# Kernel optimization log

Hardware: AMD Instinct MI355X
Metric: run time of the kernel (lower is better)

The kernel has to match this reference:

```python
import jax, jax.numpy as jnp
import numpy as np

B, N, D, H = 4, 2048, 1024, 16
DH = D // H


def setup_inputs() -> dict:
    key = jax.random.key(0)
    ks = jax.random.split(key, 9)
    s = 1.0 / np.sqrt(D)
    return {
        "x": jax.random.normal(ks[0], (B, N, D), dtype=jnp.float32),
        "Wq": jax.random.normal(ks[1], (D, D), dtype=jnp.float32) * s,
        "bq": jax.random.normal(ks[2], (D,), dtype=jnp.float32) * 0.01,
        "Wk": jax.random.normal(ks[3], (D, D), dtype=jnp.float32) * s,
        "bk": jax.random.normal(ks[4], (D,), dtype=jnp.float32) * 0.01,
        "Wv": jax.random.normal(ks[5], (D, D), dtype=jnp.float32) * s,
        "bv": jax.random.normal(ks[6], (D,), dtype=jnp.float32) * 0.01,
        "Wp": jax.random.normal(ks[7], (D, D), dtype=jnp.float32) * s,
        "bp": jax.random.normal(ks[8], (D,), dtype=jnp.float32) * 0.01,
    }


def reference(x, Wq, bq, Wk, bk, Wv, bv, Wp, bp):
    b, n, d = x.shape
    # torch Linear: x @ W.T + b; reshape to (b, h, n, dh)
    def heads(W, bias):
        y = jnp.einsum('bnd,ed->bne', x, W) + bias
        return y.reshape(b, n, H, DH).transpose(0, 2, 1, 3)
    q, k, v = heads(Wq, bq), heads(Wk, bk), heads(Wv, bv)
    # NOTE: source multiplies by sqrt(d_head) (bug in original), kept faithfully
    scale = jnp.sqrt(jnp.float32(DH))
    att = jnp.einsum('bhqd,bhkd->bhqk', q, k) * scale
    causal = jnp.triu(jnp.ones((n, n), dtype=bool), k=1)  # True above diagonal
    att = jnp.where(causal, -jnp.inf, att)
    att = jax.nn.softmax(att, axis=-1)
    # dropout is eval-mode identity
    out = jnp.einsum('bhqk,bhkd->bhqd', att, v)
    out = out.transpose(0, 2, 1, 3).reshape(b, n, d)
    return jnp.einsum('bnd,ed->bne', out, Wp) + bp
```

## Files before the change

### kernel.cpp

```cpp
#include <hip/hip_runtime.h>
#include <hip/hip_fp16.h>


typedef _Float16 half8 __attribute__((ext_vector_type(8)));
typedef _Float16 half4 __attribute__((ext_vector_type(4)));
typedef float f32x4 __attribute__((ext_vector_type(4)));
typedef unsigned int u32x4 __attribute__((ext_vector_type(4)));

#define DEV __device__ __forceinline__
#define MFMA16(a, b, c) __builtin_amdgcn_mfma_f32_16x16x32_f16(a, b, c, 0, 0, 0)

DEV void gload_lds16(const void* g, void* l) {
  __builtin_amdgcn_global_load_lds(
      (const __attribute__((address_space(1))) void*)g,
      (__attribute__((address_space(3))) void*)l, 16, 0, 0);
}

__global__ __launch_bounds__(256) void cast_all(
    const float* __restrict__ x, const float* __restrict__ Wq,
    const float* __restrict__ Wk, const float* __restrict__ Wv,
    const float* __restrict__ Wp, __half* __restrict__ xb,
    __half* __restrict__ wqkv, __half* __restrict__ wpb) {
  int i = blockIdx.x * 256 + threadIdx.x;
  const float* s;
  __half* d;
  int j;
  if (i < 1048576) {
    s = x; d = xb; j = i;
  } else {
    int k = i - 1048576;
    int sel = k >> 17;
    j = k & 131071;
    s = (sel == 0) ? Wq : (sel == 1) ? Wk : (sel == 2) ? Wv : Wp;
    d = (sel == 3) ? wpb : (wqkv + sel * 1048576);
  }
  const float4* sp = (const float4*)s + (size_t)j * 2;
  float4 a = sp[0], b = sp[1];
  half8 h;
  h[0] = (_Float16)a.x; h[1] = (_Float16)a.y; h[2] = (_Float16)a.z; h[3] = (_Float16)a.w;
  h[4] = (_Float16)b.x; h[5] = (_Float16)b.y; h[6] = (_Float16)b.z; h[7] = (_Float16)b.w;
  *((half8*)d + j) = h;
}

template <int MODE>
__global__ __launch_bounds__(256) void gemm128(
    const __half* __restrict__ A, const __half* __restrict__ Bm,
    const float* __restrict__ b0, const float* __restrict__ b1,
    const float* __restrict__ b2, __half* __restrict__ oh,
    __half* __restrict__ vtp, float* __restrict__ of) {
  const int m0 = blockIdx.y * 128;
  const int n0 = blockIdx.x * 128;
  const int tid = threadIdx.x;
  const int w = tid >> 6, lane = tid & 63;
  const int lr = lane & 15, lq = lane >> 4;
  const int wr = w >> 1, wc = w & 1;

  __shared__ alignas(16) __half As[128 * 64];
  __shared__ alignas(16) __half Bs[128 * 64];

  f32x4 acc[4][4] = {};

  const int arow = lane >> 3;
  const int acol = (lane & 7) * 8;
  const __half* Agp = A + ((size_t)m0 + w * 32 + arow) * 1024 + acol;
  const __half* Bgp = Bm + ((size_t)n0 + w * 32 + arow) * 1024 + acol;

  for (int kt = 0; kt < 16; ++kt) {
#pragma unroll
    for (int j = 0; j < 4; ++j) {
      gload_lds16(Agp + j * 8192 + kt * 64, As + (w * 4 + j) * 512);
      gload_lds16(Bgp + j * 8192 + kt * 64, Bs + (w * 4 + j) * 512);
    }
    __syncthreads();
#pragma unroll
    for (int s = 0; s < 2; ++s) {
      half8 af[4], bf[4];
#pragma unroll
      for (int i = 0; i < 4; ++i) {
        af[i] = *(const half8*)(As + (wr * 64 + i * 16 + lr) * 64 + s * 32 + lq * 8);
        bf[i] = *(const half8*)(Bs + (wc * 64 + i * 16 + lr) * 64 + s * 32 + lq * 8);
      }
#pragma unroll
      for (int mi = 0; mi < 4; ++mi)
#pragma unroll
        for (int ni = 0; ni < 4; ++ni)
          acc[mi][ni] = MFMA16(af[mi], bf[ni], acc[mi][ni]);
    }
    __syncthreads();
  }

  if (MODE == 0) {
#pragma unroll
    for (int ni = 0; ni < 4; ++ni) {
      int col = n0 + wc * 64 + ni * 16 + lr;
      int t = col >> 10, e = col & 1023;
      const float* bb = (t == 0) ? b0 : ((t == 1) ? b1 : b2);
      float bias = bb[e];
      int hh = e >> 6, dh = e & 63;
      if (t == 2) {
#pragma unroll
        for (int mi = 0; mi < 4; ++mi) {
          int row = m0 + wr * 64 + mi * 16 + lq * 4;
          int b_ = row >> 11, n = row & 2047;
          half4 h;
#pragma unroll
          for (int r = 0; r < 4; ++r) h[r] = (_Float16)(acc[mi][ni][r] + bias);
          *(half4*)(vtp + (size_t)(b_ * 16 + hh) * 131072 + (size_t)dh * 2048 + n) = h;
        }
      } else {
        float scale = (t == 0) ? 11.541560327111707f : 1.0f;
        __half* base = oh + (size_t)t * 8388608 + dh;
#pragma unroll
        for (int mi = 0; mi < 4; ++mi)
#pragma unroll
          for (int r = 0; r < 4; ++r) {
            int row = m0 + wr * 64 + mi * 16 + lq * 4 + r;
            int b_ = row >> 11, n = row & 2047;
            float v = (acc[mi][ni][r] + bias) * scale;
            base[(((size_t)(b_ * 16 + hh) * 2048 + n) * 64)] = __float2half(v);
          }
      }
    }
  } else {
#pragma unroll
    for (int ni = 0; ni < 4; ++ni) {
      int col = n0 + wc * 64 + ni * 16 + lr;
      float bias = b0[col];
#pragma unroll
      for (int mi = 0; mi < 4; ++mi)
#pragma unroll
        for (int r = 0; r < 4; ++r) {
          int row = m0 + wr * 64 + mi * 16 + lq * 4 + r;
          of[(size_t)row * 1024 + col] = acc[mi][ni][r] + bias;
        }
    }
  }
}

__global__ __launch_bounds__(256, 4) void attn128(const __half* __restrict__ Q,
                                                  const __half* __restrict__ K,
                                                  const __half* __restrict__ Vt,
                                                  __half* __restrict__ O) {
  const int wg = blockIdx.x;
  const int bh = wg & 63;
  const int a2 = wg >> 6, g4 = a2 >> 2, pos = a2 & 3;
  const int qt = (g4 == 0) ? 15 - pos
               : (g4 == 1) ? 8 + pos
               : (g4 == 2) ? 7 - pos
                           : pos;
  const int b = bh >> 4, h = bh & 15;
  const int tid = threadIdx.x;
  const int w = tid >> 6, lane = tid & 63;
  const int lr = lane & 15, lq = lane >> 4;
  const int hi = lane >> 5;
  const int sAl = (lane & 15) | ((lane & 16) << 1);
  const int sBl = sAl + 16;

  __shared__ alignas(16) __half Ks[2][4096];
  __shared__ alignas(16) __half Vs[2][4096];

  const __half* Kb = K + (size_t)bh * 131072;
  const __half* Vb = Vt + (size_t)bh * 131072;

  const int srow0 = tid >> 3;
  const int srow1 = srow0 + 32;
  const int scol = ((tid & 7) ^ (srow0 & 7)) * 8;

#define STAGE(t, buf)                                                          \
  do {                                                                         \
    gload_lds16(Kb + (size_t)((t)*64 + srow0) * 64 + scol, Ks[buf] + tid * 8); \
    gload_lds16(Kb + (size_t)((t)*64 + srow1) * 64 + scol,                     \
                Ks[buf] + 2048 + tid * 8);                                     \
    gload_lds16(Vb + (size_t)srow0 * 2048 + (t)*64 + scol, Vs[buf] + tid * 8); \
    gload_lds16(Vb + (size_t)srow1 * 2048 + (t)*64 + scol,                     \
                Vs[buf] + 2048 + tid * 8);                                     \
  } while (0)

  const int q0 = qt * 128;
  const int ktend = 2 * qt + 2;
  const int rmin = q0 + w * 32;
  const int myqa = rmin + lr;
  const int myqb = rmin + 16 + lr;

  const __half* Qpa = Q + ((size_t)bh * 2048 + rmin) * 64;
  half8 qf0a = *(const half8*)(Qpa + lr * 64 + lq * 8);
  half8 qf1a = *(const half8*)(Qpa + lr * 64 + 32 + lq * 8);
  half8 qf0b = *(const half8*)(Qpa + (16 + lr) * 64 + lq * 8);
  half8 qf1b = *(const half8*)(Qpa + (16 + lr) * 64 + 32 + lq * 8);

  f32x4 oacca[4] = {}, oaccb[4] = {};
  float ma = -INFINITY, la = 0.f, mb = -INFINITY, lb = 0.f;

  STAGE(0, 0);
  asm volatile("" ::: "memory");

  auto smgrp = [&](f32x4* sacc, float& m, float& l, int myq, int k0,
                   bool needmask, f32x4* oacc, half8& pa0, half8& pa1) {
    if (needmask) {
#pragma unroll
      for (int nt = 0; nt < 4; ++nt)
#pragma unroll
        for (int r = 0; r < 4; ++r) {
          int key = k0 + nt * 16 + lq * 4 + r;
          if (key > myq) sacc[nt][r] = -INFINITY;
        }
    }
    float rm = fmaxf(fmaxf(fmaxf(sacc[0][0], sacc[0][1]),
                           fmaxf(sacc[0][2], sacc[0][3])),
                     fmaxf(fmaxf(sacc[1][0], sacc[1][1]),
                           fmaxf(sacc[1][2], sacc[1][3])));
    rm = fmaxf(rm, fmaxf(fmaxf(fmaxf(sacc[2][0], sacc[2][1]),
                               fmaxf(sacc[2][2], sacc[2][3])),
                         fmaxf(fmaxf(sacc[3][0], sacc[3][1]),
                               fmaxf(sacc[3][2], sacc[3][3]))));
    rm = fmaxf(rm, __shfl_xor(rm, 16));
    rm = fmaxf(rm, __shfl_xor(rm, 32));
    if (__any(rm > m + 8.f)) {
      float mn = fmaxf(m, rm);
      float al = __builtin_amdgcn_exp2f(m - mn);
      m = mn;
      l *= al;
      float al4[4];
#pragma unroll
      for (int r = 0; r < 4; ++r) al4[r] = __shfl(al, lq * 4 + r);
#pragma unroll
      for (int dt = 0; dt < 4; ++dt)
#pragma unroll
        for (int r = 0; r < 4; ++r) oacc[dt][r] *= al4[r];
    }
    float ps = 0.f;
#pragma unroll
    for (int nt = 0; nt < 4; ++nt) {
      float p0 = __builtin_amdgcn_exp2f(sacc[nt][0] - m);
      float p1 = __builtin_amdgcn_exp2f(sacc[nt][1] - m);
      float p2 = __builtin_amdgcn_exp2f(sacc[nt][2] - m);
      float p3 = __builtin_amdgcn_exp2f(sacc[nt][3] - m);
      sacc[nt][0] = p0; sacc[nt][1] = p1;
      sacc[nt][2] = p2; sacc[nt][3] = p3;
      ps += (p0 + p1) + (p2 + p3);
    }
    ps += __shfl_xor(ps, 16);
    ps += __shfl_xor(ps, 32);
    l += ps;
    unsigned ph[8];
#pragma unroll
    for (int nt = 0; nt < 4; ++nt) {
      __half2 pha = __floats2half2_rn(sacc[nt][0], sacc[nt][1]);
      __half2 phb = __floats2half2_rn(sacc[nt][2], sacc[nt][3]);
      ph[2 * nt] = *(unsigned*)&pha;
      ph[2 * nt + 1] = *(unsigned*)&phb;
    }
    u32x4 fa, fb;
    {
      unsigned t0, t1;
      t0 = __shfl((int)ph[0], sAl); t1 = __shfl((int)ph[2], sAl);
      fa[0] = hi ? t1 : t0;
      t0 = __shfl((int)ph[1], sAl); t1 = __shfl((int)ph[3], sAl);
      fa[1] = hi ? t1 : t0;
      t0 = __shfl((int)ph[0], sBl); t1 = __shfl((int)ph[2], sBl);
      fa[2] = hi ? t1 : t0;
      t0 = __shfl((int)ph[1], sBl); t1 = __shfl((int)ph[3], sBl);
      fa[3] = hi ? t1 : t0;
      t0 = __shfl((int)ph[4], sAl); t1 = __shfl((int)ph[6], sAl);
      fb[0] = hi ? t1 : t0;
      t0 = __shfl((int)ph[5], sAl); t1 = __shfl((int)ph[7], sAl);
      fb[1] = hi ? t1 : t0;
      t0 = __shfl((int)ph[4], sBl); t1 = __shfl((int)ph[6], sBl);
      fb[2] = hi ? t1 : t0;
      t0 = __shfl((int)ph[5], sBl); t1 = __shfl((int)ph[7], sBl);
      fb[3] = hi ? t1 : t0;
    }
    pa0 = *(half8*)&fa;
    pa1 = *(half8*)&fb;
  };

  for (int kt = 0; kt < ktend; ++kt) {
    const int cur = kt & 1;
    const int k0 = kt * 64;
    if (kt + 1 < ktend) {
      STAGE(kt + 1, cur ^ 1);
      asm volatile("s_waitcnt vmcnt(4)" ::: "memory");
    } else {
      asm volatile("s_waitcnt vmcnt(0)" ::: "memory");
    }
    __builtin_amdgcn_s_barrier();
    asm volatile("" ::: "memory");

    const char* Kc = (const char*)Ks[cur];
    const char* Vc = (const char*)Vs[cur];
    if (k0 <= rmin + 31) {
      f32x4 sa[4] = {}, sb[4] = {};
      __builtin_amdgcn_s_setprio(1);
#pragma unroll
      for (int nt = 0; nt < 4; ++nt) {
        int row = nt * 16 + lr;
        half8 kb0 = *(const half8*)(Kc + ((row * 128 + lq * 16) ^ ((row & 7) << 4)));
        half8 kb1 = *(const half8*)(Kc + ((row * 128 + 64 + lq * 16) ^ ((row & 7) << 4)));
        sa[nt] = MFMA16(kb0, qf0a, sa[nt]);
        sa[nt] = MFMA16(kb1, qf1a, sa[nt]);
        sb[nt] = MFMA16(kb0, qf0b, sb[nt]);
        sb[nt] = MFMA16(kb1, qf1b, sb[nt]);
      }
      __builtin_amdgcn_s_setprio(0);

      half8 paa0, paa1, pab0, pab1;
      smgrp(sa, ma, la, myqa, k0, k0 + 63 > rmin, oacca, paa0, paa1);
      smgrp(sb, mb, lb, myqb, k0, k0 + 63 > rmin + 16, oaccb, pab0, pab1);

      __builtin_amdgcn_s_setprio(1);
#pragma unroll
      for (int dt = 0; dt < 4; ++dt) {
        int row = dt * 16 + lr;
        half8 vb0 = *(const half8*)(Vc + ((row * 128 + lq * 16) ^ ((row & 7) << 4)));
        half8 vb1 = *(const half8*)(Vc + ((row * 128 + 64 + lq * 16) ^ ((row & 7) << 4)));
        oacca[dt] = MFMA16(paa0, vb0, oacca[dt]);
        oacca[dt] = MFMA16(paa1, vb1, oacca[dt]);
        oaccb[dt] = MFMA16(pab0, vb0, oaccb[dt]);
        oaccb[dt] = MFMA16(pab1, vb1, oaccb[dt]);
      }
      __builtin_amdgcn_s_setprio(0);
    }
    asm volatile("s_waitcnt lgkmcnt(0)" ::: "memory");
    __builtin_amdgcn_s_barrier();
    asm volatile("" ::: "memory");
  }

  float linva = 1.0f / la, linvb = 1.0f / lb;
  float inva[4], invb[4];
#pragma unroll
  for (int r = 0; r < 4; ++r) {
    inva[r] = __shfl(linva, lq * 4 + r);
    invb[r] = __shfl(linvb, lq * 4 + r);
  }
  __half* Opa = O + ((size_t)b * 2048 + rmin) * 1024 + h * 64;
#pragma unroll
  for (int dt = 0; dt < 4; ++dt)
#pragma unroll
    for (int r = 0; r < 4; ++r) {
      Opa[(size_t)(lq * 4 + r) * 1024 + dt * 16 + lr] =
          __float2half(oacca[dt][r] * inva[r]);
      Opa[(size_t)(16 + lq * 4 + r) * 1024 + dt * 16 + lr] =
          __float2half(oaccb[dt][r] * invb[r]);
    }
#undef STAGE
}

extern "C" void kernel_launch(void* const* d_in, const int* in_sizes, int n_in,
                              void* d_out, int out_size, void* d_ws,
                              size_t ws_size, hipStream_t stream) {
  const float* x = (const float*)d_in[0];
  const float* Wq = (const float*)d_in[1];
  const float* bq = (const float*)d_in[2];
  const float* Wk = (const float*)d_in[3];
  const float* bk = (const float*)d_in[4];
  const float* Wv = (const float*)d_in[5];
  const float* bv = (const float*)d_in[6];
  const float* Wp = (const float*)d_in[7];
  const float* bp = (const float*)d_in[8];

  char* ws = (char*)d_ws;
  const size_t XB = 0;
  const size_t WQKV = XB + 16777216;
  const size_t WPB = WQKV + 6291456;
  const size_t QKV = WPB + 2097152;
  const size_t VT = QKV + 50331648;
  const size_t OB = VT + 16777216;

  __half* xb = (__half*)(ws + XB);
  __half* wqkv = (__half*)(ws + WQKV);
  __half* wpb = (__half*)(ws + WPB);
  __half* qkv = (__half*)(ws + QKV);
  __half* vt = (__half*)(ws + VT);
  __half* ob = (__half*)(ws + OB);

  cast_all<<<6144, 256, 0, stream>>>(x, Wq, Wk, Wv, Wp, xb, wqkv, wpb);

  gemm128<0><<<dim3(24, 64), 256, 0, stream>>>(xb, wqkv, bq, bk, bv, qkv, vt,
                                               nullptr);
  attn128<<<dim3(1024), 256, 0, stream>>>(qkv, qkv + 8388608, vt, ob);
  gemm128<1><<<dim3(8, 64), 256, 0, stream>>>(ob, wpb, bp, nullptr, nullptr,
                                              nullptr, nullptr, (float*)d_out);
}
```

Before: 190.8 us.

## Widen attention waves to 64 query rows with 128-thread blocks

The attention kernel now uses 2-wave, 128-thread blocks, and each wave processes 64 query rows as four 16-row groups instead of 32 rows. This doubles the reuse of each K/V fragment read from LDS, and each thread stages twice as many K/V chunks. Groups lying entirely above the causal diagonal skip their MFMAs and softmax. The row-sum cross-lane reduction moves from every tile to the epilogue. The interleaved query-tile schedule is replaced by a plain heavy-first order, and the larger per-wave accumulator state raises register pressure and may lower occupancy.

```diff
diff --git a/kernel.cpp b/kernel.cpp
--- a/kernel.cpp
+++ b/kernel.cpp
@@ -137,17 +137,12 @@
   }
 }
 
-__global__ __launch_bounds__(256, 4) void attn128(const __half* __restrict__ Q,
-                                                  const __half* __restrict__ K,
-                                                  const __half* __restrict__ Vt,
-                                                  __half* __restrict__ O) {
+__global__ __launch_bounds__(128, 2) void attn_quad(
+    const __half* __restrict__ Q, const __half* __restrict__ K,
+    const __half* __restrict__ Vt, __half* __restrict__ O) {
   const int wg = blockIdx.x;
   const int bh = wg & 63;
-  const int a2 = wg >> 6, g4 = a2 >> 2, pos = a2 & 3;
-  const int qt = (g4 == 0) ? 15 - pos
-               : (g4 == 1) ? 8 + pos
-               : (g4 == 2) ? 7 - pos
-                           : pos;
+  const int qt = 15 - (wg >> 6);
   const int b = bh >> 4, h = bh & 15;
   const int tid = threadIdx.x;
   const int w = tid >> 6, lane = tid & 63;
@@ -162,34 +157,40 @@
   const __half* Kb = K + (size_t)bh * 131072;
   const __half* Vb = Vt + (size_t)bh * 131072;
 
-  const int srow0 = tid >> 3;
-  const int srow1 = srow0 + 32;
-  const int scol = ((tid & 7) ^ (srow0 & 7)) * 8;
+  const int srow = tid >> 3;
+  const int scol = ((tid & 7) ^ (srow & 7)) * 8;
 
 #define STAGE(t, buf)                                                          \
   do {                                                                         \
-    gload_lds16(Kb + (size_t)((t)*64 + srow0) * 64 + scol, Ks[buf] + tid * 8); \
-    gload_lds16(Kb + (size_t)((t)*64 + srow1) * 64 + scol,                     \
-                Ks[buf] + 2048 + tid * 8);                                     \
-    gload_lds16(Vb + (size_t)srow0 * 2048 + (t)*64 + scol, Vs[buf] + tid * 8); \
-    gload_lds16(Vb + (size_t)srow1 * 2048 + (t)*64 + scol,                     \
-                Vs[buf] + 2048 + tid * 8);                                     \
+    const __half* kg = Kb + (size_t)((t)*64 + srow) * 64 + scol;               \
+    const __half* vg = Vb + (size_t)srow * 2048 + (t)*64 + scol;               \
+    gload_lds16(kg, Ks[buf] + tid * 8);                                        \
+    gload_lds16(kg + 16 * 64, Ks[buf] + 1024 + tid * 8);                       \
+    gload_lds16(kg + 32 * 64, Ks[buf] + 2048 + tid * 8);                       \
+    gload_lds16(kg + 48 * 64, Ks[buf] + 3072 + tid * 8);                       \
+    gload_lds16(vg, Vs[buf] + tid * 8);                                        \
+    gload_lds16(vg + 16 * 2048, Vs[buf] + 1024 + tid * 8);                     \
+    gload_lds16(vg + 32 * 2048, Vs[buf] + 2048 + tid * 8);                     \
+    gload_lds16(vg + 48 * 2048, Vs[buf] + 3072 + tid * 8);                     \
   } while (0)
 
   const int q0 = qt * 128;
   const int ktend = 2 * qt + 2;
-  const int rmin = q0 + w * 32;
-  const int myqa = rmin + lr;
-  const int myqb = rmin + 16 + lr;
+  const int rmin = q0 + w * 64;
 
   const __half* Qpa = Q + ((size_t)bh * 2048 + rmin) * 64;
   half8 qf0a = *(const half8*)(Qpa + lr * 64 + lq * 8);
   half8 qf1a = *(const half8*)(Qpa + lr * 64 + 32 + lq * 8);
   half8 qf0b = *(const half8*)(Qpa + (16 + lr) * 64 + lq * 8);
   half8 qf1b = *(const half8*)(Qpa + (16 + lr) * 64 + 32 + lq * 8);
-
-  f32x4 oacca[4] = {}, oaccb[4] = {};
+  half8 qf0c = *(const half8*)(Qpa + (32 + lr) * 64 + lq * 8);
+  half8 qf1c = *(const half8*)(Qpa + (32 + lr) * 64 + 32 + lq * 8);
+  half8 qf0d = *(const half8*)(Qpa + (48 + lr) * 64 + lq * 8);
+  half8 qf1d = *(const half8*)(Qpa + (48 + lr) * 64 + 32 + lq * 8);
+
+  f32x4 oacca[4] = {}, oaccb[4] = {}, oaccc[4] = {}, oaccd[4] = {};
   float ma = -INFINITY, la = 0.f, mb = -INFINITY, lb = 0.f;
+  float mc = -INFINITY, lc = 0.f, md = -INFINITY, ld = 0.f;
 
   STAGE(0, 0);
   asm volatile("" ::: "memory");
@@ -239,8 +240,6 @@
       sacc[nt][2] = p2; sacc[nt][3] = p3;
       ps += (p0 + p1) + (p2 + p3);
     }
-    ps += __shfl_xor(ps, 16);
-    ps += __shfl_xor(ps, 32);
     l += ps;
     unsigned ph[8];
 #pragma unroll
@@ -279,7 +278,7 @@
     const int k0 = kt * 64;
     if (kt + 1 < ktend) {
       STAGE(kt + 1, cur ^ 1);
-      asm volatile("s_waitcnt vmcnt(4)" ::: "memory");
+      asm volatile("s_waitcnt vmcnt(8)" ::: "memory");
     } else {
       asm volatile("s_waitcnt vmcnt(0)" ::: "memory");
     }
@@ -288,24 +287,29 @@
 
     const char* Kc = (const char*)Ks[cur];
     const char* Vc = (const char*)Vs[cur];
-    if (k0 <= rmin + 31) {
-      f32x4 sa[4] = {}, sb[4] = {};
+    if (k0 <= rmin + 63) {
+      const bool acta = (k0 <= rmin + 15);
+      const bool actb = (k0 <= rmin + 31);
+      const bool actc = (k0 <= rmin + 47);
+      f32x4 sa[4] = {}, sb[4] = {}, sc[4] = {}, sd[4] = {};
       __builtin_amdgcn_s_setprio(1);
 #pragma unroll
       for (int nt = 0; nt < 4; ++nt) {
         int row = nt * 16 + lr;
         half8 kb0 = *(const half8*)(Kc + ((row * 128 + lq * 16) ^ ((row & 7) << 4)));
         half8 kb1 = *(const half8*)(Kc + ((row * 128 + 64 + lq * 16) ^ ((row & 7) << 4)));
-        sa[nt] = MFMA16(kb0, qf0a, sa[nt]);
-        sa[nt] = MFMA16(kb1, qf1a, sa[nt]);
-        sb[nt] = MFMA16(kb0, qf0b, sb[nt]);
-        sb[nt] = MFMA16(kb1, qf1b, sb[nt]);
+        if (acta) { sa[nt] = MFMA16(kb0, qf0a, sa[nt]); sa[nt] = MFMA16(kb1, qf1a, sa[nt]); }
+        if (actb) { sb[nt] = MFMA16(kb0, qf0b, sb[nt]); sb[nt] = MFMA16(kb1, qf1b, sb[nt]); }
+        if (actc) { sc[nt] = MFMA16(kb0, qf0c, sc[nt]); sc[nt] = MFMA16(kb1, qf1c, sc[nt]); }
+        sd[nt] = MFMA16(kb0, qf0d, sd[nt]); sd[nt] = MFMA16(kb1, qf1d, sd[nt]);
       }
       __builtin_amdgcn_s_setprio(0);
 
-      half8 paa0, paa1, pab0, pab1;
-      smgrp(sa, ma, la, myqa, k0, k0 + 63 > rmin, oacca, paa0, paa1);
-      smgrp(sb, mb, lb, myqb, k0, k0 + 63 > rmin + 16, oaccb, pab0, pab1);
+      half8 paa0, paa1, pab0, pab1, pac0, pac1, pad0, pad1;
+      if (acta) smgrp(sa, ma, la, rmin + lr, k0, k0 + 63 > rmin, oacca, paa0, paa1);
+      if (actb) smgrp(sb, mb, lb, rmin + 16 + lr, k0, k0 + 63 > rmin + 16, oaccb, pab0, pab1);
+      if (actc) smgrp(sc, mc, lc, rmin + 32 + lr, k0, k0 + 63 > rmin + 32, oaccc, pac0, pac1);
+      smgrp(sd, md, ld, rmin + 48 + lr, k0, k0 + 63 > rmin + 48, oaccd, pad0, pad1);
 
       __builtin_amdgcn_s_setprio(1);
 #pragma unroll
@@ -313,10 +317,10 @@
         int row = dt * 16 + lr;
         half8 vb0 = *(const half8*)(Vc + ((row * 128 + lq * 16) ^ ((row & 7) << 4)));
         half8 vb1 = *(const half8*)(Vc + ((row * 128 + 64 + lq * 16) ^ ((row & 7) << 4)));
-        oacca[dt] = MFMA16(paa0, vb0, oacca[dt]);
-        oacca[dt] = MFMA16(paa1, vb1, oacca[dt]);
-        oaccb[dt] = MFMA16(pab0, vb0, oaccb[dt]);
-        oaccb[dt] = MFMA16(pab1, vb1, oaccb[dt]);
+        if (acta) { oacca[dt] = MFMA16(paa0, vb0, oacca[dt]); oacca[dt] = MFMA16(paa1, vb1, oacca[dt]); }
+        if (actb) { oaccb[dt] = MFMA16(pab0, vb0, oaccb[dt]); oaccb[dt] = MFMA16(pab1, vb1, oaccb[dt]); }
+        if (actc) { oaccc[dt] = MFMA16(pac0, vb0, oaccc[dt]); oaccc[dt] = MFMA16(pac1, vb1, oaccc[dt]); }
+        oaccd[dt] = MFMA16(pad0, vb0, oaccd[dt]); oaccd[dt] = MFMA16(pad1, vb1, oaccd[dt]);
       }
       __builtin_amdgcn_s_setprio(0);
     }
@@ -325,23 +329,26 @@
     asm volatile("" ::: "memory");
   }
 
-  float linva = 1.0f / la, linvb = 1.0f / lb;
-  float inva[4], invb[4];
-#pragma unroll
-  for (int r = 0; r < 4; ++r) {
-    inva[r] = __shfl(linva, lq * 4 + r);
-    invb[r] = __shfl(linvb, lq * 4 + r);
-  }
-  __half* Opa = O + ((size_t)b * 2048 + rmin) * 1024 + h * 64;
-#pragma unroll
-  for (int dt = 0; dt < 4; ++dt)
-#pragma unroll
-    for (int r = 0; r < 4; ++r) {
-      Opa[(size_t)(lq * 4 + r) * 1024 + dt * 16 + lr] =
-          __float2half(oacca[dt][r] * inva[r]);
-      Opa[(size_t)(16 + lq * 4 + r) * 1024 + dt * 16 + lr] =
-          __float2half(oaccb[dt][r] * invb[r]);
-    }
+  auto epi = [&](f32x4* oacc, float lpart, int grow) {
+    float lt = lpart;
+    lt += __shfl_xor(lt, 16);
+    lt += __shfl_xor(lt, 32);
+    float linv = 1.0f / lt;
+    float inv4[4];
+#pragma unroll
+    for (int r = 0; r < 4; ++r) inv4[r] = __shfl(linv, lq * 4 + r);
+    __half* Op = O + ((size_t)b * 2048 + rmin + grow) * 1024 + h * 64;
+#pragma unroll
+    for (int dt = 0; dt < 4; ++dt)
+#pragma unroll
+      for (int r = 0; r < 4; ++r)
+        Op[(size_t)(lq * 4 + r) * 1024 + dt * 16 + lr] =
+            __float2half(oacc[dt][r] * inv4[r]);
+  };
+  epi(oacca, la, 0);
+  epi(oaccb, lb, 16);
+  epi(oaccc, lc, 32);
+  epi(oaccd, ld, 48);
 #undef STAGE
 }
 
@@ -377,7 +384,7 @@
 
   gemm128<0><<<dim3(24, 64), 256, 0, stream>>>(xb, wqkv, bq, bk, bv, qkv, vt,
                                                nullptr);
-  attn128<<<dim3(1024), 256, 0, stream>>>(qkv, qkv + 8388608, vt, ob);
+  attn_quad<<<dim3(1024), 128, 0, stream>>>(qkv, qkv + 8388608, vt, ob);
   gemm128<1><<<dim3(8, 64), 256, 0, stream>>>(ob, wpb, bp, nullptr, nullptr,
                                               nullptr, nullptr, (float*)d_out);
 }
```

After: 230.3 us. 1.21x slower.
